# Performance work log

Measured on AMD Instinct MI355X. Metric: run time of the kernel, lower is better.

Reference implementation:

```python
import jax, jax.numpy as jnp
import numpy as np

N = 16384

def setup_inputs() -> dict:
    key = jax.random.key(0)
    k1, k2 = jax.random.split(key)
    predict = jax.random.normal(k1, (N,), dtype=jnp.float32)
    target = jax.random.normal(k2, (N,), dtype=jnp.float32)
    return {"predict": predict, "target": target}

def reference(predict, target):
    n = predict.shape[0]
    # hardtanh(predict[i]-predict[j]) * hardtanh(target[i]-target[j]) summed over i>j.
    # The product matrix is symmetric with zero diagonal, so the strict lower-
    # triangular sum equals half the full-matrix sum.
    pd = jnp.clip(predict[:, None] - predict[None, :], -1.0, 1.0)  # [N, N]
    td = jnp.clip(target[:, None] - target[None, :], -1.0, 1.0)   # [N, N]
    full_sum = jnp.sum(pd * td)
    num = full_sum * 0.5
    denom = jnp.asarray(n * (n - 1), dtype=predict.dtype)
    return 1.0 - 2.0 * num / denom
```

## Files before the change

kernel.cpp:

```cpp
#include <hip/hip_runtime.h>

#define BLOCK 512
#define IPT   4
#define ITILE 2048
#define JS    128
#define JT_PER_I 16
#define NT    576
#define RBLOCK 1024

__global__ __launch_bounds__(BLOCK) void kendall_pairs(
    const float* __restrict__ p, const float* __restrict__ t,
    float* __restrict__ partial, int n) {
    __shared__ float2 sj[JS];

    const int s = blockIdx.x;
    int bi = (int)((__builtin_sqrtf(4.0f + 2.0f * (float)s) - 2.0f) * 0.25f);
    while (8 * (bi + 1) * (bi + 2) <= s) ++bi;
    while (8 * bi * (bi + 1) > s) --bi;
    const int bj = s - 8 * bi * (bi + 1);
    const float w = (bj < JT_PER_I * bi) ? 2.0f : 1.0f;

    if (threadIdx.x < JS) {
        int j = bj * JS + threadIdx.x;
        sj[threadIdx.x] = make_float2(p[j], t[j]);
    }

    float2 pit[IPT];
#pragma unroll
    for (int u = 0; u < IPT; ++u) {
        int i = bi * ITILE + u * BLOCK + threadIdx.x;
        pit[u] = make_float2(p[i], t[i]);
    }
    __syncthreads();

    float a[2 * IPT] = {0.0f};
    const float4* j4 = reinterpret_cast<const float4*>(sj);
#pragma unroll 4
    for (int g = 0; g < JS / 2; ++g) {
        float4 jv = j4[g];
#pragma unroll
        for (int u = 0; u < IPT; ++u) {
            float pd0 = __builtin_amdgcn_fmed3f(pit[u].x - jv.x, -1.0f, 1.0f);
            float td0 = __builtin_amdgcn_fmed3f(pit[u].y - jv.y, -1.0f, 1.0f);
            a[2 * u]     = fmaf(pd0, td0, a[2 * u]);
            float pd1 = __builtin_amdgcn_fmed3f(pit[u].x - jv.z, -1.0f, 1.0f);
            float td1 = __builtin_amdgcn_fmed3f(pit[u].y - jv.w, -1.0f, 1.0f);
            a[2 * u + 1] = fmaf(pd1, td1, a[2 * u + 1]);
        }
    }

    float r = ((a[0] + a[1]) + (a[2] + a[3])) + ((a[4] + a[5]) + (a[6] + a[7]));
#pragma unroll
    for (int off = 32; off > 0; off >>= 1) r += __shfl_down(r, off, 64);

    if ((threadIdx.x & 63) == 0)
        partial[blockIdx.x * (BLOCK / 64) + (threadIdx.x >> 6)] = w * r;
}

__global__ __launch_bounds__(RBLOCK) void kendall_reduce(
    const float* __restrict__ partial, float* __restrict__ out,
    int nPartial, int n) {
    __shared__ float wsum[RBLOCK / 64];
    float s = 0.0f;
    for (int k = threadIdx.x; k < nPartial; k += RBLOCK) s += partial[k];
#pragma unroll
    for (int off = 32; off > 0; off >>= 1) s += __shfl_down(s, off, 64);
    const int lane = threadIdx.x & 63;
    const int wid  = threadIdx.x >> 6;
    if (lane == 0) wsum[wid] = s;
    __syncthreads();
    if (threadIdx.x == 0) {
        float S = 0.0f;
#pragma unroll
        for (int v2 = 0; v2 < RBLOCK / 64; ++v2) S += wsum[v2];
        float denom = (float)n * (float)(n - 1);
        out[0] = 1.0f - S / denom;
    }
}

extern "C" void kernel_launch(void* const* d_in, const int* in_sizes, int n_in,
                              void* d_out, int out_size, void* d_ws, size_t ws_size,
                              hipStream_t stream) {
    const float* predict = (const float*)d_in[0];
    const float* target  = (const float*)d_in[1];
    float* out = (float*)d_out;
    float* partial = (float*)d_ws;
    const int n = in_sizes[0];

    const int nPartial = NT * (BLOCK / 64);
    kendall_pairs<<<NT, BLOCK, 0, stream>>>(predict, target, partial, n);
    kendall_reduce<<<1, RBLOCK, 0, stream>>>(partial, out, nPartial, n);
}
```

Baseline: 79.07 us.

## Compute pairwise clipped differences in packed fp16 with fdot2 accumulation

Converts predict/target values to half precision, stores j-tile values as packed half2 in shared memory, and computes differences and clamps with packed fp16 min/max, accumulating the products with v_dot2 into fp32. This halves the number of ALU instructions per pair. The trade-off is reduced precision: fp16 rounding of inputs and differences introduces error into the summed statistic, which may exceed tolerance.

Result: faster. 77.19 us (median of 2 runs) (-2.4%).

```diff
diff --git a/kernel.cpp b/kernel.cpp
--- a/kernel.cpp
+++ b/kernel.cpp
@@ -8,10 +8,13 @@
 #define NT    576
 #define RBLOCK 1024
 
+typedef _Float16 h2 __attribute__((ext_vector_type(2)));
+
 __global__ __launch_bounds__(BLOCK) void kendall_pairs(
     const float* __restrict__ p, const float* __restrict__ t,
     float* __restrict__ partial, int n) {
-    __shared__ float2 sj[JS];
+    __shared__ unsigned int sjp[JS / 2];
+    __shared__ unsigned int sjt[JS / 2];
 
     const int s = blockIdx.x;
     int bi = (int)((__builtin_sqrtf(4.0f + 2.0f * (float)s) - 2.0f) * 0.25f);
@@ -21,35 +24,55 @@
     const float w = (bj < JT_PER_I * bi) ? 2.0f : 1.0f;
 
     if (threadIdx.x < JS) {
-        int j = bj * JS + threadIdx.x;
-        sj[threadIdx.x] = make_float2(p[j], t[j]);
+        const int k = threadIdx.x & 63;
+        const float2* src = (const float2*)((threadIdx.x < 64 ? p : t) + bj * JS);
+        float2 v = src[k];
+        h2 hv = {(_Float16)v.x, (_Float16)v.y};
+        unsigned int bitsv; __builtin_memcpy(&bitsv, &hv, 4);
+        (threadIdx.x < 64 ? sjp : sjt)[k] = bitsv;
     }
 
-    float2 pit[IPT];
+    h2 pi2[IPT], ti2[IPT];
 #pragma unroll
     for (int u = 0; u < IPT; ++u) {
         int i = bi * ITILE + u * BLOCK + threadIdx.x;
-        pit[u] = make_float2(p[i], t[i]);
+        _Float16 ph = (_Float16)p[i];
+        _Float16 th = (_Float16)t[i];
+        pi2[u] = (h2){ph, ph};
+        ti2[u] = (h2){th, th};
     }
     __syncthreads();
 
-    float a[2 * IPT] = {0.0f};
-    const float4* j4 = reinterpret_cast<const float4*>(sj);
+    const h2 neg1 = {(_Float16)-1.0f, (_Float16)-1.0f};
+    const h2 pos1 = {(_Float16)1.0f, (_Float16)1.0f};
+
+    float acc[IPT] = {0.0f};
+    const uint4* jp4 = (const uint4*)sjp;
+    const uint4* jt4 = (const uint4*)sjt;
+
 #pragma unroll 4
-    for (int g = 0; g < JS / 2; ++g) {
-        float4 jv = j4[g];
+    for (int g = 0; g < JS / 8; ++g) {
+        uint4 jp = jp4[g];
+        uint4 jt = jt4[g];
+        unsigned int jpw[4] = {jp.x, jp.y, jp.z, jp.w};
+        unsigned int jtw[4] = {jt.x, jt.y, jt.z, jt.w};
 #pragma unroll
-        for (int u = 0; u < IPT; ++u) {
-            float pd0 = __builtin_amdgcn_fmed3f(pit[u].x - jv.x, -1.0f, 1.0f);
-            float td0 = __builtin_amdgcn_fmed3f(pit[u].y - jv.y, -1.0f, 1.0f);
-            a[2 * u]     = fmaf(pd0, td0, a[2 * u]);
-            float pd1 = __builtin_amdgcn_fmed3f(pit[u].x - jv.z, -1.0f, 1.0f);
-            float td1 = __builtin_amdgcn_fmed3f(pit[u].y - jv.w, -1.0f, 1.0f);
-            a[2 * u + 1] = fmaf(pd1, td1, a[2 * u + 1]);
+        for (int c = 0; c < 4; ++c) {
+            h2 pj, tj;
+            __builtin_memcpy(&pj, &jpw[c], 4);
+            __builtin_memcpy(&tj, &jtw[c], 4);
+#pragma unroll
+            for (int u = 0; u < IPT; ++u) {
+                h2 pd = __builtin_elementwise_min(
+                            __builtin_elementwise_max(pi2[u] - pj, neg1), pos1);
+                h2 td = __builtin_elementwise_min(
+                            __builtin_elementwise_max(ti2[u] - tj, neg1), pos1);
+                acc[u] = __builtin_amdgcn_fdot2(pd, td, acc[u], false);
+            }
         }
     }
 
-    float r = ((a[0] + a[1]) + (a[2] + a[3])) + ((a[4] + a[5]) + (a[6] + a[7]));
+    float r = (acc[0] + acc[1]) + (acc[2] + acc[3]);
 #pragma unroll
     for (int off = 32; off > 0; off >>= 1) r += __shfl_down(r, off, 64);
 
```
